# Kernel tuning notes

Hardware: AMD Instinct MI355X
Metric: run time of the kernel (lower is better)

The kernel has to match this reference:

```python
import jax, jax.numpy as jnp
import numpy as np

B, S, T = 32, 128, 64
H = 512
VS = VT = 32000


def _lstm_cell(x, h, c, W, U, b):
    # Keras LSTM gate order: i, f, g(cell), o
    z = x @ W + h @ U + b
    i, f, g, o = jnp.split(z, 4, axis=-1)
    c = jax.nn.sigmoid(f) * c + jax.nn.sigmoid(i) * jnp.tanh(g)
    h = jax.nn.sigmoid(o) * jnp.tanh(c)
    return h, c


def _lstm_scan(xs, h0, c0, W, U, b):
    # xs: [S, B, D]
    def step(carry, x):
        h, c = _lstm_cell(x, carry[0], carry[1], W, U, b)
        return (h, c), h
    (hT, cT), hs = jax.lax.scan(step, (h0, c0), xs)
    return hs, hT, cT


def setup_inputs() -> dict:
    key = jax.random.key(0)
    ks = jax.random.split(key, 16)
    def n(k, shape, s=0.02):
        return (jax.random.normal(k, shape, jnp.float32) * s).astype(jnp.float32)
    return {
        "src": jax.random.randint(ks[0], (B, S), 0, VS, jnp.int32),
        "trg": jax.random.randint(ks[1], (B, T), 0, VT, jnp.int32),
        "E_src": n(ks[2], (VS, H)),
        "E_trg": n(ks[3], (VT, H)),
        "Wf": n(ks[4], (H, 4 * H)), "Uf": n(ks[5], (H, 4 * H)), "bf": jnp.zeros((4 * H,), jnp.float32),
        "Wb": n(ks[6], (H, 4 * H)), "Ub": n(ks[7], (H, 4 * H)), "bb": jnp.zeros((4 * H,), jnp.float32),
        "Wd": n(ks[8], (H, 4 * H)), "Ud": n(ks[9], (H, 4 * H)), "bd": jnp.zeros((4 * H,), jnp.float32),
        "fcW": n(ks[10], (2 * H, H)), "fcb": jnp.zeros((H,), jnp.float32),
        "clsW": n(ks[11], (2 * H, VT)), "clsb": jnp.zeros((VT,), jnp.float32),
    }


def reference(src, trg, E_src, E_trg, Wf, Uf, bf, Wb, Ub, bb, Wd, Ud, bd, fcW, fcb, clsW, clsb):
    Bn = src.shape[0]
    Hn = E_src.shape[1]
    # --- Encoder: bidirectional LSTM ---
    xs = E_src[src].transpose(1, 0, 2)          # [S, B, H]
    z0 = jnp.zeros((Bn, Hn), xs.dtype)
    hs_f, hf, cf = _lstm_scan(xs, z0, z0, Wf, Uf, bf)
    hs_b, hb, cb = _lstm_scan(xs[::-1], z0, z0, Wb, Ub, bb)
    src_hidden = jnp.concatenate([hs_f, hs_b[::-1]], axis=-1).transpose(1, 0, 2)  # [B, S, 2H]
    # --- shared fc projections (same Dense, 2H -> H) ---
    src_h = src_hidden @ fcW + fcb                                   # [B, S, H]
    prev_h = jnp.concatenate([hf, hb], axis=-1) @ fcW + fcb          # [B, H]
    prev_c = jnp.concatenate([cf, cb], axis=-1) @ fcW + fcb          # [B, H]
    neg = jnp.where(src == 0, jnp.float32(-1e9), jnp.float32(0.0))   # [B, S]
    # --- Decoder (teacher forcing): per-step LSTM cell + dot-product attention ---
    ys = E_trg[trg[:, :-1]].transpose(1, 0, 2)  # [T-1, B, H]

    def step(carry, x):
        h, c = _lstm_cell(x, carry[0], carry[1], Wd, Ud, bd)
        score = jnp.einsum('bh,bsh->bs', h, src_h) + neg
        attn = jax.nn.softmax(score, axis=-1)
        ws = jnp.einsum('bs,bsh->bh', attn, src_h)
        return (h, c), jnp.concatenate([ws, h], axis=-1)  # dec_state [B, 2H]

    _, dec = jax.lax.scan(step, (prev_h, prev_c), ys)     # [T-1, B, 2H]
    logits = dec.transpose(1, 0, 2) @ clsW + clsb          # [B, T-1, VT]
    return logits
```

## Files before the change

### kernel.cpp

```cpp
#include <hip/hip_runtime.h>
#include <hip/hip_bf16.h>
#include <stdint.h>
#include <string.h>

constexpr int cB = 32, cS = 128, cT = 64, cH = 512, cH4 = 2048, cVT = 32000, cTM1 = 63;

typedef __attribute__((ext_vector_type(8))) __bf16 bf16x8;
typedef __attribute__((ext_vector_type(4))) float f32x4;

__device__ __forceinline__ float sigm(float x) { return 1.0f / (1.0f + expf(-x)); }

__device__ __forceinline__ bf16x8 sc_load16(const __hip_bfloat16* p) {
  bf16x8 r;
  asm volatile("global_load_dwordx4 %0, %1, off sc0 sc1"
               : "=&v"(r) : "v"(p) : "memory");
  return r;
}
__device__ __forceinline__ void sc_store4(__hip_bfloat16* p, unsigned v) {
  asm volatile("global_store_dword %0, %1, off sc0 sc1"
               :: "v"(p), "v"(v) : "memory");
}
__device__ __forceinline__ void pl_store4(__hip_bfloat16* p, unsigned v) {
  asm volatile("global_store_dword %0, %1, off"
               :: "v"(p), "v"(v) : "memory");
}
__device__ __forceinline__ unsigned sc_loadu(const unsigned* p) {
  unsigned r;
  asm volatile("global_load_dword %0, %1, off sc0 sc1"
               : "=&v"(r) : "v"(p) : "memory");
  asm volatile("s_waitcnt vmcnt(0)" ::: "memory");
  return r;
}
__device__ __forceinline__ void sc_storeu(unsigned* p, unsigned v) {
  asm volatile("global_store_dword %0, %1, off sc0 sc1"
               :: "v"(p), "v"(v) : "memory");
}

__global__ __launch_bounds__(64) void k_init_bars(unsigned* p) {
  p[threadIdx.x] = 0u;
}

__global__ __launch_bounds__(128) void k_embed_src(const int* __restrict__ src,
                                                   const float* __restrict__ E,
                                                   __hip_bfloat16* __restrict__ xs_bf,
                                                   float* __restrict__ neg) {
  int sb = blockIdx.x;
  int s = sb >> 5, b = sb & 31;
  int tok = src[b * cS + s];
  float4 e = ((const float4*)(E + (size_t)tok * cH))[threadIdx.x];
  __hip_bfloat16* drow = xs_bf + (size_t)sb * cH + threadIdx.x * 4;
  drow[0] = __float2bfloat16(e.x); drow[1] = __float2bfloat16(e.y);
  drow[2] = __float2bfloat16(e.z); drow[3] = __float2bfloat16(e.w);
  if (threadIdx.x == 0) neg[b * cS + s] = (tok == 0) ? -1e9f : 0.0f;
}

__global__ __launch_bounds__(128) void k_embed_trg(const int* __restrict__ trg,
                                                   const float* __restrict__ E,
                                                   __hip_bfloat16* __restrict__ ys_bf) {
  int tb = blockIdx.x;
  int t = tb >> 5, b = tb & 31;
  int tok = trg[b * cT + t];
  float4 e = ((const float4*)(E + (size_t)tok * cH))[threadIdx.x];
  __hip_bfloat16* drow = ys_bf + (size_t)tb * cH + threadIdx.x * 4;
  drow[0] = __float2bfloat16(e.x); drow[1] = __float2bfloat16(e.y);
  drow[2] = __float2bfloat16(e.z); drow[3] = __float2bfloat16(e.w);
}

__device__ __forceinline__ void f2bT_tile(const float* __restrict__ src,
                                          __hip_bfloat16* __restrict__ dst,
                                          int K, int N, int gi, int bx, int by,
                                          float (*t)[33]) {
  int nt = bx * 32, kt = by * 32;
  int c = threadIdx.x & 31, r0 = threadIdx.x >> 5;
#pragma unroll
  for (int i = 0; i < 4; ++i) {
    int r = r0 + i * 8;
    t[r][c] = src[(size_t)(kt + r) * N + nt + c];
  }
  __syncthreads();
#pragma unroll
  for (int i = 0; i < 4; ++i) {
    int row = nt + r0 + i * 8;
    int pr = gi ? (((row & 511) << 2) | (row >> 9)) : row;
    dst[(size_t)pr * K + kt + c] = __float2bfloat16(t[c][r0 + i * 8]);
  }
  __syncthreads();
}

__device__ __forceinline__ void f2bT_tile512(const float* __restrict__ src,
                                             __hip_bfloat16* __restrict__ dst,
                                             int K, int N, int bx, int by,
                                             float (*t)[33]) {
  int nt = bx * 32, kt = by * 32;
  int c = threadIdx.x & 31, r0 = (threadIdx.x >> 5) & 15;
#pragma unroll
  for (int i = 0; i < 2; ++i) {
    int r = r0 + i * 16;
    t[r][c] = src[(size_t)(kt + r) * N + nt + c];
  }
  __syncthreads();
#pragma unroll
  for (int i = 0; i < 2; ++i) {
    int row = nt + r0 + i * 16;
    dst[(size_t)row * K + kt + c] = __float2bfloat16(t[c][r0 + i * 16]);
  }
  __syncthreads();
}

__global__ __launch_bounds__(256) void k_prep(
    const float* __restrict__ Wf, const float* __restrict__ Wb, const float* __restrict__ Wd,
    const float* __restrict__ Uf, const float* __restrict__ Ub, const float* __restrict__ Ud,
    const float* __restrict__ fcW,
    const float* __restrict__ bf, const float* __restrict__ bb, const float* __restrict__ bd,
    __hip_bfloat16* __restrict__ Wtfx, __hip_bfloat16* __restrict__ Wtbx,
    __hip_bfloat16* __restrict__ Wtdx,
    __hip_bfloat16* __restrict__ Utf, __hip_bfloat16* __restrict__ Utb,
    __hip_bfloat16* __restrict__ Utd,
    __hip_bfloat16* __restrict__ fcWt,
    float* __restrict__ bfx, float* __restrict__ bbx, float* __restrict__ bdx,
    __hip_bfloat16* __restrict__ ys_pad) {
  __shared__ float t[32][33];
  int id = blockIdx.x;
  if (id < 6144) {
    int grp = id >> 10, r = id & 1023;
    const float* s; __hip_bfloat16* d;
    switch (grp) {
      case 0: s = Wf; d = Wtfx; break;
      case 1: s = Wb; d = Wtbx; break;
      case 2: s = Wd; d = Wtdx; break;
      case 3: s = Uf; d = Utf; break;
      case 4: s = Ub; d = Utb; break;
      default: s = Ud; d = Utd; break;
    }
    f2bT_tile(s, d, 512, 2048, 1, r & 63, r >> 6, t);
  } else if (id < 6656) {
    int r = id - 6144;
    f2bT_tile(fcW, fcWt, 1024, 512, 0, r & 15, r >> 4, t);
  } else if (id < 6680) {
    int r = id - 6656;
    const float* s = (r < 8) ? bf : ((r < 16) ? bb : bd);
    float* d = (r < 8) ? bfx : ((r < 16) ? bbx : bdx);
    int i = (r & 7) * 256 + threadIdx.x;
    d[i] = s[(i & 3) * 512 + (i >> 2)];
  } else {
    int r = id - 6680;
    ys_pad[r * 256 + threadIdx.x] = __float2bfloat16(0.0f);
  }
}

__global__ __launch_bounds__(256) void k_bgemm(const __hip_bfloat16* __restrict__ A,
                                               const __hip_bfloat16* __restrict__ Bt,
                                               const float* __restrict__ bias,
                                               float* __restrict__ C,
                                               int M, int K, int N) {
  __shared__ __hip_bfloat16 As[128 * 64];
  __shared__ __hip_bfloat16 Bs[128 * 64];
  const int tid = threadIdx.x;
  const int lane = tid & 63;
  const int wave = tid >> 6;
  const int wr = wave >> 1, wc = wave & 1;
  const int bm = blockIdx.x * 128, bn = blockIdx.y * 128;

  f32x4 acc[4][4] = {};

  const int srow = lane >> 3;
  const int scol = (lane & 7) * 8;

  for (int kt = 0; kt < K; kt += 64) {
#pragma unroll
    for (int i = 0; i < 4; ++i) {
      int c = wave * 4 + i;
      const __hip_bfloat16* ga = A + (size_t)(bm + c * 8 + srow) * K + kt + scol;
      __builtin_amdgcn_global_load_lds(
          (const __attribute__((address_space(1))) uint32_t*)ga,
          (__attribute__((address_space(3))) uint32_t*)(As + c * 512), 16, 0, 0);
      const __hip_bfloat16* gb = Bt + (size_t)(bn + c * 8 + srow) * K + kt + scol;
      __builtin_amdgcn_global_load_lds(
          (const __attribute__((address_space(1))) uint32_t*)gb,
          (__attribute__((address_space(3))) uint32_t*)(Bs + c * 512), 16, 0, 0);
    }
    __syncthreads();

#pragma unroll
    for (int kk = 0; kk < 64; kk += 32) {
      const int ko = kk + (lane >> 4) * 8;
      bf16x8 a[4], b[4];
      const int ar = wr * 64 + (lane & 15);
#pragma unroll
      for (int m = 0; m < 4; ++m)
        a[m] = *(const bf16x8*)(As + (size_t)(ar + m * 16) * 64 + ko);
      const int br = wc * 64 + (lane & 15);
#pragma unroll
      for (int n = 0; n < 4; ++n)
        b[n] = *(const bf16x8*)(Bs + (size_t)(br + n * 16) * 64 + ko);
#pragma unroll
      for (int m = 0; m < 4; ++m)
#pragma unroll
        for (int n = 0; n < 4; ++n)
          acc[m][n] = __builtin_amdgcn_mfma_f32_16x16x32_bf16(a[m], b[n], acc[m][n], 0, 0, 0);
    }
    __syncthreads();
  }

#pragma unroll
  for (int m = 0; m < 4; ++m) {
    const int row0 = bm + wr * 64 + m * 16 + (lane >> 4) * 4;
#pragma unroll
    for (int n = 0; n < 4; ++n) {
      const int col = bn + wc * 64 + n * 16 + (lane & 15);
      const float bv = bias[col];
#pragma unroll
      for (int r = 0; r < 4; ++r) {
        const int row = row0 + r;
        if (row < M) C[(size_t)row * N + col] = acc[m][n][r] + bv;
      }
    }
  }
}

#define SLOT_BARRIER(SLOTS, NB, GEN)                                             \
  {                                                                              \
    asm volatile("s_waitcnt vmcnt(2)" ::: "memory");                             \
    __builtin_amdgcn_sched_barrier(0);                                           \
    __builtin_amdgcn_s_barrier();                                                \
    if (tid == 0) sc_storeu((SLOTS) + (NB), (unsigned)(GEN));                    \
    if (wv == 0) {                                                               \
      for (;;) {                                                                 \
        unsigned v = sc_loadu((SLOTS) + (lane & 15));                            \
        if (__all((lane >= 16) | (v >= (unsigned)(GEN)))) break;                 \
        __builtin_amdgcn_s_sleep(1);                                             \
      }                                                                          \
    }                                                                            \
    __builtin_amdgcn_s_barrier();                                                \
    __builtin_amdgcn_sched_barrier(0);                                           \
  }

#define ENC_STEP(T, ZI0, ZI1, ZO0, ZO1)                                          \
  {                                                                              \
    const int t = (T);                                                           \
    const int trow = dir ? (127 - t) : t;                                        \
    if (t > 0) {                                                                 \
      const __hip_bfloat16* hsrc = hcur + (size_t)((t + 1) & 1) * 16384;         \
      bf16x8 hr[4];                                                              \
      _Pragma("unroll")                                                          \
      for (int i = 0; i < 4; ++i) {                                              \
        int c = tid + i * 512;                                                   \
        hr[i] = sc_load16(hsrc + (size_t)c * 8);                                 \
      }                                                                          \
      asm volatile("s_waitcnt vmcnt(0)" ::: "memory");                           \
      __builtin_amdgcn_sched_barrier(0);                                         \
      _Pragma("unroll")                                                          \
      for (int i = 0; i < 4; ++i) {                                              \
        int c = tid + i * 512;                                                   \
        int r = c >> 6, cc = (c & 63) * 8;                                       \
        *(bf16x8*)&Hs[r][cc] = hr[i];                                            \
      }                                                                          \
      asm volatile("s_waitcnt lgkmcnt(0)" ::: "memory");                         \
      __builtin_amdgcn_s_barrier();                                              \
      __builtin_amdgcn_sched_barrier(0);                                         \
    }                                                                            \
    f32x4 acc0 = {}, acc1 = {};                                                  \
    if (t > 0) {                                                                 \
      _Pragma("unroll")                                                          \
      for (int kk = 0; kk < 16; ++kk) {                                          \
        bf16x8 h0v = *(const bf16x8*)&Hs[b0][kk * 32 + fq * 8];                  \
        bf16x8 h1v = *(const bf16x8*)&Hs[b1][kk * 32 + fq * 8];                  \
        acc0 = __builtin_amdgcn_mfma_f32_16x16x32_bf16(afrag[kk], h0v, acc0, 0, 0, 0); \
        acc1 = __builtin_amdgcn_mfma_f32_16x16x32_bf16(afrag[kk], h1v, acc1, 0, 0, 0); \
      }                                                                          \
    }                                                                            \
    {                                                                            \
      float zi = ZI0[0] + acc0[0], zf = ZI0[1] + acc0[1],                        \
            zg = ZI0[2] + acc0[2], zo = ZI0[3] + acc0[3];                        \
      cs0 = sigm(zf) * cs0 + sigm(zi) * tanhf(zg);                               \
      Ho[b0][jloc] = __float2bfloat16(sigm(zo) * tanhf(cs0));                    \
    }                                                                            \
    {                                                                            \
      float zi = ZI1[0] + acc1[0], zf = ZI1[1] + acc1[1],                        \
            zg = ZI1[2] + acc1[2], zo = ZI1[3] + acc1[3];                        \
      cs1 = sigm(zf) * cs1 + sigm(zi) * tanhf(zg);                               \
      Ho[b1][jloc] = __float2bfloat16(sigm(zo) * tanhf(cs1));                    \
    }                                                                            \
    asm volatile("s_waitcnt lgkmcnt(0)" ::: "memory");                           \
    __builtin_amdgcn_s_barrier();                                                \
    __builtin_amdgcn_sched_barrier(0);                                           \
    {                                                                            \
      unsigned v = *(const unsigned*)&Ho[bb][jp];                                \
      sc_store4(hcur + (size_t)(t & 1) * 16384 + (size_t)bb * 512 + nb * 32 + jp, v); \
      pl_store4(hs + ((size_t)trow * 32 + bb) * 512 + nb * 32 + jp, v);          \
    }                                                                            \
    __builtin_amdgcn_sched_barrier(0);                                           \
    const int tn = (t < 127) ? t + 1 : 127;                                      \
    const int ntrow = dir ? (127 - tn) : tn;                                     \
    ZO0 = *(const f32x4*)(xW + ((size_t)(ntrow * 32 + b0)) * 2048 + zc);         \
    ZO1 = *(const f32x4*)(xW + ((size_t)(ntrow * 32 + b1)) * 2048 + zc);         \
    if (t < 127) SLOT_BARRIER(slots, nb, t + 1);                                 \
  }

__global__ __launch_bounds__(512, 1) void k_enc_mfma(
    const float* __restrict__ xWf, const float* __restrict__ xWb,
    const __hip_bfloat16* __restrict__ Utf, const __hip_bfloat16* __restrict__ Utb,
    __hip_bfloat16* __restrict__ hs_f, __hip_bfloat16* __restrict__ hs_b,
    __hip_bfloat16* __restrict__ henc,
    float* __restrict__ cf, float* __restrict__ cb,
    unsigned* bars) {
  __shared__ __hip_bfloat16 Hs[32][520];
  __shared__ __hip_bfloat16 Ho[32][36];

  const int bid = blockIdx.x;
  const int dir = bid >> 4, nb = bid & 15;
  const int c0 = nb * 128;
  const float* xW = dir ? xWb : xWf;
  const __hip_bfloat16* Ut = dir ? Utb : Utf;
  __hip_bfloat16* hs = dir ? hs_b : hs_f;
  __hip_bfloat16* hcur = henc + (size_t)dir * 32768;
  float* cOut = dir ? cb : cf;
  unsigned* slots = bars + dir * 16;

  const int tid = threadIdx.x;
  const int lane = tid & 63;
  const int wv = tid >> 6;
  const int fr = lane & 15;
  const int fq = lane >> 4;

  bf16x8 afrag[16];
#pragma unroll
  for (int kk = 0; kk < 16; ++kk)
    afrag[kk] = *(const bf16x8*)(Ut + (size_t)(c0 + wv * 16 + fr) * 512 + kk * 32 + fq * 8);

  const int jglob = nb * 32 + wv * 4 + fq;
  const int jloc = wv * 4 + fq;
  const int b0 = fr, b1 = fr + 16;
  const int zc = c0 + wv * 16 + fq * 4;
  const int bb = tid >> 4, jp = (tid & 15) * 2;
  float cs0 = 0.f, cs1 = 0.f;

  const int trow0 = dir ? 127 : 0;
  f32x4 zA0 = *(const f32x4*)(xW + ((size_t)(trow0 * 32 + b0)) * 2048 + zc);
  f32x4 zA1 = *(const f32x4*)(xW + ((size_t)(trow0 * 32 + b1)) * 2048 + zc);
  f32x4 zB0, zB1;

  for (int it = 0; it < 64; ++it) {
    ENC_STEP(2 * it, zA0, zA1, zB0, zB1);
    ENC_STEP(2 * it + 1, zB0, zB1, zA0, zA1);
  }
  cOut[(size_t)b0 * 512 + jglob] = cs0;
  cOut[(size_t)b1 * 512 + jglob] = cs1;
}

#define DEC_STEP(T, ZI0, ZI1, ZO0, ZO1)                                          \
  {                                                                              \
    const int t = (T);                                                           \
    if (t == 0) {                                                                \
      const float4* ph4 = (const float4*)prev_h;                                 \
      _Pragma("unroll")                                                          \
      for (int i = 0; i < 8; ++i) {                                              \
        int c = tid + i * 512;                                                   \
        float4 v = ph4[c];                                                       \
        int r = c >> 7, c4 = (c & 127) * 4;                                      \
        Hs[r][c4 + 0] = __float2bfloat16(v.x);                                   \
        Hs[r][c4 + 1] = __float2bfloat16(v.y);                                   \
        Hs[r][c4 + 2] = __float2bfloat16(v.z);                                   \
        Hs[r][c4 + 3] = __float2bfloat16(v.w);                                   \
      }                                                                          \
    } else {                                                                     \
      const __hip_bfloat16* hsrc = hdec + (size_t)((t + 1) & 1) * 16384;         \
      bf16x8 hr[4];                                                              \
      _Pragma("unroll")                                                          \
      for (int i = 0; i < 4; ++i) {                                              \
        int c = tid + i * 512;                                                   \
        hr[i] = sc_load16(hsrc + (size_t)c * 8);                                 \
      }                                                                          \
      asm volatile("s_waitcnt vmcnt(0)" ::: "memory");                           \
      __builtin_amdgcn_sched_barrier(0);                                         \
      _Pragma("unroll")                                                          \
      for (int i = 0; i < 4; ++i) {                                              \
        int c = tid + i * 512;                                                   \
        int r = c >> 6, cc = (c & 63) * 8;                                       \
        *(bf16x8*)&Hs[r][cc] = hr[i];                                            \
      }                                                                          \
    }                                                                            \
    asm volatile("s_waitcnt lgkmcnt(0)" ::: "memory");                           \
    __builtin_amdgcn_s_barrier();                                                \
    __builtin_amdgcn_sched_barrier(0);                                           \
    f32x4 acc0 = {}, acc1 = {};                                                  \
    _Pragma("unroll")                                                            \
    for (int kk = 0; kk < 16; ++kk) {                                            \
      bf16x8 h0v = *(const bf16x8*)&Hs[b0][kk * 32 + fq * 8];                    \
      bf16x8 h1v = *(const bf16x8*)&Hs[b1][kk * 32 + fq * 8];                    \
      acc0 = __builtin_amdgcn_mfma_f32_16x16x32_bf16(afrag[kk], h0v, acc0, 0, 0, 0); \
      acc1 = __builtin_amdgcn_mfma_f32_16x16x32_bf16(afrag[kk], h1v, acc1, 0, 0, 0); \
    }                                                                            \
    {                                                                            \
      float zi = ZI0[0] + acc0[0], zf = ZI0[1] + acc0[1],                        \
            zg = ZI0[2] + acc0[2], zo = ZI0[3] + acc0[3];                        \
      cs0 = sigm(zf) * cs0 + sigm(zi) * tanhf(zg);                               \
      Ho[b0][jloc] = __float2bfloat16(sigm(zo) * tanhf(cs0));                    \
    }                                                                            \
    {                                                                            \
      float zi = ZI1[0] + acc1[0], zf = ZI1[1] + acc1[1],                        \
            zg = ZI1[2] + acc1[2], zo = ZI1[3] + acc1[3];                        \
      cs1 = sigm(zf) * cs1 + sigm(zi) * tanhf(zg);                               \
      Ho[b1][jloc] = __float2bfloat16(sigm(zo) * tanhf(cs1));                    \
    }                                                                            \
    asm volatile("s_waitcnt lgkmcnt(0)" ::: "memory");                           \
    __builtin_amdgcn_s_barrier();                                                \
    __builtin_amdgcn_sched_barrier(0);                                           \
    {                                                                            \
      unsigned v = *(const unsigned*)&Ho[bb][jp];                                \
      sc_store4(hdec + (size_t)(t & 1) * 16384 + (size_t)bb * 512 + nb * 32 + jp, v); \
      pl_store4(decb + ((size_t)bb * cTM1 + t) * 1024 + 512 + nb * 32 + jp, v);  \
    }                                                                            \
    __builtin_amdgcn_sched_barrier(0);                                           \
    const int tn = (t < cTM1 - 1) ? t + 1 : cTM1 - 1;                            \
    ZO0 = *(const f32x4*)(yW + ((size_t)(tn * 32 + b0)) * 2048 + zc);            \
    ZO1 = *(const f32x4*)(yW + ((size_t)(tn * 32 + b1)) * 2048 + zc);            \
    if (t < cTM1 - 1) SLOT_BARRIER(slots, nb, t + 1);                            \
  }

__global__ __launch_bounds__(512, 1) void k_dec_mfma(
    const float* __restrict__ yW, const __hip_bfloat16* __restrict__ Utd,
    const float* __restrict__ prev_h, const float* __restrict__ prev_c,
    __hip_bfloat16* __restrict__ hdec, __hip_bfloat16* __restrict__ decb,
    const float* __restrict__ clsW, __hip_bfloat16* __restrict__ clsWt,
    unsigned* slots) {
  __shared__ __hip_bfloat16 Hs[32][520];
  __shared__ __hip_bfloat16 Ho[32][36];
  __shared__ float tcv[32][33];

  if (blockIdx.x >= 16) {
    for (int tile = blockIdx.x - 16; tile < 32000; tile += (int)gridDim.x - 16) {
      int bx = tile % 1000, by = tile / 1000;
      f2bT_tile512(clsW, clsWt, 1024, 32000, bx, by, tcv);
    }
    return;
  }

  const int nb = blockIdx.x;
  const int c0 = nb * 128;
  const int tid = threadIdx.x;
  const int lane = tid & 63;
  const int wv = tid >> 6;
  const int fr = lane & 15;
  const int fq = lane >> 4;

  bf16x8 afrag[16];
#pragma unroll
  for (int kk = 0; kk < 16; ++kk)
    afrag[kk] = *(const bf16x8*)(Utd + (size_t)(c0 + wv * 16 + fr) * 512 + kk * 32 + fq * 8);

  const int jglob = nb * 32 + wv * 4 + fq;
  const int jloc = wv * 4 + fq;
  const int b0 = fr, b1 = fr + 16;
  const int zc = c0 + wv * 16 + fq * 4;
  const int bb = tid >> 4, jp = (tid & 15) * 2;
  float cs0 = prev_c[(size_t)b0 * 512 + jglob];
  float cs1 = prev_c[(size_t)b1 * 512 + jglob];

  f32x4 zA0 = *(const f32x4*)(yW + ((size_t)b0) * 2048 + zc);
  f32x4 zA1 = *(const f32x4*)(yW + ((size_t)b1) * 2048 + zc);
  f32x4 zB0, zB1;

  for (int it = 0; it < 31; ++it) {
    DEC_STEP(2 * it, zA0, zA1, zB0, zB1);
    DEC_STEP(2 * it + 1, zB0, zB1, zA0, zA1);
  }
  DEC_STEP(62, zA0, zA1, zB0, zB1);
}

__global__ __launch_bounds__(128) void k_cat_bf(const __hip_bfloat16* __restrict__ hs_f,
                                                const __hip_bfloat16* __restrict__ hs_b,
                                                const float* __restrict__ cf,
                                                const float* __restrict__ cb,
                                                __hip_bfloat16* __restrict__ cat) {
  int r = blockIdx.x;
  int tid = threadIdx.x;
  __hip_bfloat16* drow = cat + (size_t)r * 1024 + tid * 8;
  if (r >= 4160) {
    bf16x8 zv = {};
    *(bf16x8*)drow = zv;
    return;
  }
  if (r < 4128) {
    const __hip_bfloat16 *pf, *pb;
    if (r < 4096) {
      int b = r >> 7, s = r & 127;
      pf = hs_f + ((size_t)s * 32 + b) * 512;
      pb = hs_b + ((size_t)s * 32 + b) * 512;
    } else {
      int b = r - 4096;
      pf = hs_f + ((size_t)127 * 32 + b) * 512;
      pb = hs_b + ((size_t)b) * 512;
    }
    const __hip_bfloat16* s8 = (tid < 64) ? (pf + tid * 8) : (pb + (tid - 64) * 8);
    *(bf16x8*)drow = *(const bf16x8*)s8;
  } else {
    int b = r - 4128;
    const float* s8 = (tid < 64) ? (cf + (size_t)b * 512 + tid * 8)
                                 : (cb + (size_t)b * 512 + (tid - 64) * 8);
    bf16x8 v;
#pragma unroll
    for (int i = 0; i < 8; ++i) v[i] = (__bf16)s8[i];
    *(bf16x8*)drow = v;
  }
}

__global__ __launch_bounds__(256) void k_attn_all(const float* __restrict__ src_h,
                                                  const float* __restrict__ neg,
                                                  __hip_bfloat16* __restrict__ decb) {
  int bid = blockIdx.x;
  int xcd = bid & 7, idx = bid >> 3;
  int b = xcd + 8 * (idx / 63);
  int t = idx % 63;
  int tx = threadIdx.x;
  __shared__ float hv[cH];
  __shared__ float part[256];
  __shared__ float sc[cS];
  __shared__ float red[cS];
  __hip_bfloat16* drow = decb + ((size_t)b * cTM1 + t) * (2 * cH);
  hv[tx] = __bfloat162float(drow[cH + tx]);
  hv[tx + 256] = __bfloat162float(drow[cH + tx + 256]);
  __syncthreads();
  {
    int s = tx >> 1, half = tx & 1;
    const float4* sr = (const float4*)(src_h + ((size_t)b * cS + s) * cH + half * 256);
    const float4* hh = (const float4*)(hv + half * 256);
    float acc = 0.f;
#pragma unroll 8
    for (int k = 0; k < 64; ++k) {
      float4 v = sr[k], h4 = hh[k];
      acc += v.x * h4.x + v.y * h4.y + v.z * h4.z + v.w * h4.w;
    }
    part[tx] = acc;
  }
  __syncthreads();
  if (tx < cS) {
    float s0 = part[2 * tx] + part[2 * tx + 1] + neg[b * cS + tx];
    sc[tx] = s0;
    red[tx] = s0;
  }
  __syncthreads();
  for (int off = 64; off >= 1; off >>= 1) {
    if (tx < off) red[tx] = fmaxf(red[tx], red[tx + off]);
    __syncthreads();
  }
  float mx = red[0];
  __syncthreads();
  float e = 0.f;
  if (tx < cS) { e = expf(sc[tx] - mx); red[tx] = e; }
  __syncthreads();
  for (int off = 64; off >= 1; off >>= 1) {
    if (tx < off) red[tx] += red[tx + off];
    __syncthreads();
  }
  float inv = 1.0f / red[0];
  __syncthreads();
  if (tx < cS) sc[tx] = e * inv;
  __syncthreads();
  float a0 = 0.f, a1 = 0.f;
  for (int s = 0; s < cS; ++s) {
    float w = sc[s];
    const float* sr = src_h + ((size_t)b * cS + s) * cH;
    a0 += w * sr[tx];
    a1 += w * sr[tx + 256];
  }
  drow[tx] = __float2bfloat16(a0);
  drow[tx + 256] = __float2bfloat16(a1);
}

extern "C" void kernel_launch(void* const* d_in, const int* in_sizes, int n_in,
                              void* d_out, int out_size, void* d_ws, size_t ws_size,
                              hipStream_t stream) {
  const int* src = (const int*)d_in[0];
  const int* trg = (const int*)d_in[1];
  const float* E_src = (const float*)d_in[2];
  const float* E_trg = (const float*)d_in[3];
  const float* Wf = (const float*)d_in[4];
  const float* Uf = (const float*)d_in[5];
  const float* bf = (const float*)d_in[6];
  const float* Wb = (const float*)d_in[7];
  const float* Ub = (const float*)d_in[8];
  const float* bb = (const float*)d_in[9];
  const float* Wd = (const float*)d_in[10];
  const float* Ud = (const float*)d_in[11];
  const float* bd = (const float*)d_in[12];
  const float* fcW = (const float*)d_in[13];
  const float* fcb = (const float*)d_in[14];
  const float* clsW = (const float*)d_in[15];
  const float* clsb = (const float*)d_in[16];
  float* out = (float*)d_out;
  float* ws = (float*)d_ws;

  float* xWf = ws;
  float* xWb = ws + 8388608;
  float* yW = ws + 16777216;
  __hip_bfloat16* hs_f = (__hip_bfloat16*)(ws + 20905984);
  __hip_bfloat16* hs_b = (__hip_bfloat16*)(ws + 21954560);
  float* cf = ws + 23003136;
  float* cb = ws + 23019520;
  float* neg = ws + 23035904;
  float* fco = ws + 23040000;
  __hip_bfloat16* decb = (__hip_bfloat16*)(ws + 25169920);
  __hip_bfloat16* Utd = (__hip_bfloat16*)(ws + 26218496);
  __hip_bfloat16* henc = (__hip_bfloat16*)(ws + 26742784);
  __hip_bfloat16* hdec = (__hip_bfloat16*)(ws + 26808320);
  unsigned* bars = (unsigned*)(ws + 26841088);
  float* pool = ws + 26841152;

  __hip_bfloat16* xs_bf = (__hip_bfloat16*)pool;
  __hip_bfloat16* ys_bf = (__hip_bfloat16*)(pool + 1048576);
  __hip_bfloat16* Utf = (__hip_bfloat16*)(pool + 1572864);
  __hip_bfloat16* Utb = (__hip_bfloat16*)(pool + 2097152);
  __hip_bfloat16* Wtfx = (__hip_bfloat16*)(pool + 2621440);
  __hip_bfloat16* Wtbx = (__hip_bfloat16*)(pool + 3145728);
  __hip_bfloat16* Wtdx = (__hip_bfloat16*)(pool + 3670016);
  float* bfx = pool + 4194304;
  float* bbx = pool + 4196352;
  float* bdx = pool + 4198400;
  __hip_bfloat16* fcWt = (__hip_bfloat16*)(pool + 4200448);
  __hip_bfloat16* cat_bf = (__hip_bfloat16*)pool;
  __hip_bfloat16* clsWt = (__hip_bfloat16*)xWf;

  k_embed_src<<<4096, 128, 0, stream>>>(src, E_src, xs_bf, neg);
  k_embed_trg<<<2016, 128, 0, stream>>>(trg, E_trg, ys_bf);
  k_prep<<<6744, 256, 0, stream>>>(Wf, Wb, Wd, Uf, Ub, Ud, fcW, bf, bb, bd,
                                   Wtfx, Wtbx, Wtdx, Utf, Utb, Utd, fcWt,
                                   bfx, bbx, bdx, ys_bf + (size_t)2016 * 512);

  k_bgemm<<<dim3(32, 16), 256, 0, stream>>>(xs_bf, Wtfx, bfx, xWf, 4096, 512, 2048);
  k_bgemm<<<dim3(32, 16), 256, 0, stream>>>(xs_bf, Wtbx, bbx, xWb, 4096, 512, 2048);
  k_bgemm<<<dim3(16, 16), 256, 0, stream>>>(ys_bf, Wtdx, bdx, yW, 2016, 512, 2048);

  k_init_bars<<<1, 64, 0, stream>>>(bars);
  k_enc_mfma<<<32, 512, 0, stream>>>(xWf, xWb, Utf, Utb, hs_f, hs_b, henc, cf, cb, bars);

  k_cat_bf<<<4224, 128, 0, stream>>>(hs_f, hs_b, cf, cb, cat_bf);
  k_bgemm<<<dim3(33, 4), 256, 0, stream>>>(cat_bf, fcWt, fcb, fco, 4160, 1024, 512);

  const float* prev_h = fco + (size_t)4096 * 512;
  const float* prev_c = fco + (size_t)4128 * 512;
  k_dec_mfma<<<256, 512, 0, stream>>>(yW, Utd, prev_h, prev_c, hdec, decb,
                                      clsW, clsWt, bars + 32);
  k_attn_all<<<2016, 256, 0, stream>>>(fco, neg, decb);

  k_bgemm<<<dim3(16, 250), 256, 0, stream>>>(decb, clsWt, clsb, out, 2016, 1024, 32000);
}
```

Measured before the change: 1.208 ms.

## Overlap decoder attention with recurrence and write encoder states straight into concat buffer

The encoder now stores each hidden state directly into the [B,S,2H] concatenated bf16 buffer, so the full k_cat_bf repack is replaced by a small tail kernel that handles only the final-state rows. The separate attention kernel is removed. After the 240 spare blocks of the decoder kernel finish transposing the classifier weights, they poll the per-step slot counters and compute attention for each (t,b) as soon as that step's hidden state is published. This hides attention behind the serial decoder recurrence, at the cost of coherent sc0/sc1 stores for decoder outputs, spin-waiting, and a narrower per-block attention loop.

```diff
diff --git a/kernel.cpp b/kernel.cpp
--- a/kernel.cpp
+++ b/kernel.cpp
@@ -13,6 +13,12 @@
 __device__ __forceinline__ bf16x8 sc_load16(const __hip_bfloat16* p) {
   bf16x8 r;
   asm volatile("global_load_dwordx4 %0, %1, off sc0 sc1"
+               : "=&v"(r) : "v"(p) : "memory");
+  return r;
+}
+__device__ __forceinline__ unsigned sc_load4u(const __hip_bfloat16* p) {
+  unsigned r;
+  asm volatile("global_load_dword %0, %1, off sc0 sc1"
                : "=&v"(r) : "v"(p) : "memory");
   return r;
 }
@@ -287,7 +293,7 @@
     {                                                                            \
       unsigned v = *(const unsigned*)&Ho[bb][jp];                                \
       sc_store4(hcur + (size_t)(t & 1) * 16384 + (size_t)bb * 512 + nb * 32 + jp, v); \
-      pl_store4(hs + ((size_t)trow * 32 + bb) * 512 + nb * 32 + jp, v);          \
+      pl_store4(catb + ((size_t)(bb * 128 + trow)) * 1024 + dhalf + nb * 32 + jp, v); \
     }                                                                            \
     __builtin_amdgcn_sched_barrier(0);                                           \
     const int tn = (t < 127) ? t + 1 : 127;                                      \
@@ -300,7 +306,7 @@
 __global__ __launch_bounds__(512, 1) void k_enc_mfma(
     const float* __restrict__ xWf, const float* __restrict__ xWb,
     const __hip_bfloat16* __restrict__ Utf, const __hip_bfloat16* __restrict__ Utb,
-    __hip_bfloat16* __restrict__ hs_f, __hip_bfloat16* __restrict__ hs_b,
+    __hip_bfloat16* __restrict__ catb,
     __hip_bfloat16* __restrict__ henc,
     float* __restrict__ cf, float* __restrict__ cb,
     unsigned* bars) {
@@ -312,7 +318,7 @@
   const int c0 = nb * 128;
   const float* xW = dir ? xWb : xWf;
   const __hip_bfloat16* Ut = dir ? Utb : Utf;
-  __hip_bfloat16* hs = dir ? hs_b : hs_f;
+  const int dhalf = dir * 512;
   __hip_bfloat16* hcur = henc + (size_t)dir * 32768;
   float* cOut = dir ? cb : cf;
   unsigned* slots = bars + dir * 16;
@@ -346,6 +352,62 @@
   }
   cOut[(size_t)b0 * 512 + jglob] = cs0;
   cOut[(size_t)b1 * 512 + jglob] = cs1;
+}
+
+__device__ void attn_one(const float* __restrict__ src_h, const float* __restrict__ neg,
+                         __hip_bfloat16* __restrict__ decb, int b, int t,
+                         float* hv, float* sc, float* red) {
+  const int tx = threadIdx.x;
+  __hip_bfloat16* drow = decb + ((size_t)b * cTM1 + t) * 1024;
+  if (tx < 256) {
+    unsigned u = sc_load4u(drow + 512 + tx * 2);
+    asm volatile("s_waitcnt vmcnt(0)" ::: "memory");
+    hv[tx * 2] = __uint_as_float(u << 16);
+    hv[tx * 2 + 1] = __uint_as_float(u & 0xffff0000u);
+  }
+  __syncthreads();
+  {
+    int s = tx >> 2, q = tx & 3;
+    const float4* sr = (const float4*)(src_h + ((size_t)b * cS + s) * cH + q * 128);
+    const float4* hh = (const float4*)(hv + q * 128);
+    float acc = 0.f;
+#pragma unroll 8
+    for (int k = 0; k < 32; ++k) {
+      float4 v = sr[k], h4 = hh[k];
+      acc += v.x * h4.x + v.y * h4.y + v.z * h4.z + v.w * h4.w;
+    }
+    acc += __shfl_xor(acc, 1);
+    acc += __shfl_xor(acc, 2);
+    if (q == 0) {
+      float s0 = acc + neg[b * cS + s];
+      sc[s] = s0;
+      red[s] = s0;
+    }
+  }
+  __syncthreads();
+  for (int off = 64; off >= 1; off >>= 1) {
+    if (tx < off) red[tx] = fmaxf(red[tx], red[tx + off]);
+    __syncthreads();
+  }
+  float mx = red[0];
+  __syncthreads();
+  float e = 0.f;
+  if (tx < cS) { e = expf(sc[tx] - mx); red[tx] = e; }
+  __syncthreads();
+  for (int off = 64; off >= 1; off >>= 1) {
+    if (tx < off) red[tx] += red[tx + off];
+    __syncthreads();
+  }
+  float inv = 1.0f / red[0];
+  __syncthreads();
+  if (tx < cS) sc[tx] = e * inv;
+  __syncthreads();
+  {
+    float a = 0.f;
+    const float* sr = src_h + (size_t)b * cS * cH + tx;
+    for (int s = 0; s < cS; ++s) a += sc[s] * sr[(size_t)s * cH];
+    drow[tx] = __float2bfloat16(a);
+  }
 }
 
 #define DEC_STEP(T, ZI0, ZI1, ZO0, ZO1)                                          \
@@ -409,7 +471,7 @@
     {                                                                            \
       unsigned v = *(const unsigned*)&Ho[bb][jp];                                \
       sc_store4(hdec + (size_t)(t & 1) * 16384 + (size_t)bb * 512 + nb * 32 + jp, v); \
-      pl_store4(decb + ((size_t)bb * cTM1 + t) * 1024 + 512 + nb * 32 + jp, v);  \
+      sc_store4(decb + ((size_t)bb * cTM1 + t) * 1024 + 512 + nb * 32 + jp, v);  \
     }                                                                            \
     __builtin_amdgcn_sched_barrier(0);                                           \
     const int tn = (t < cTM1 - 1) ? t + 1 : cTM1 - 1;                            \
@@ -423,24 +485,46 @@
     const float* __restrict__ prev_h, const float* __restrict__ prev_c,
     __hip_bfloat16* __restrict__ hdec, __hip_bfloat16* __restrict__ decb,
     const float* __restrict__ clsW, __hip_bfloat16* __restrict__ clsWt,
+    const float* __restrict__ src_h, const float* __restrict__ neg,
     unsigned* slots) {
   __shared__ __hip_bfloat16 Hs[32][520];
   __shared__ __hip_bfloat16 Ho[32][36];
   __shared__ float tcv[32][33];
-
-  if (blockIdx.x >= 16) {
-    for (int tile = blockIdx.x - 16; tile < 32000; tile += (int)gridDim.x - 16) {
-      int bx = tile % 1000, by = tile / 1000;
-      f2bT_tile512(clsW, clsWt, 1024, 32000, bx, by, tcv);
-    }
-    return;
-  }
-
-  const int nb = blockIdx.x;
-  const int c0 = nb * 128;
+  __shared__ float hv_sh[512];
+  __shared__ float sc_sh[128];
+  __shared__ float red_sh[128];
+
   const int tid = threadIdx.x;
   const int lane = tid & 63;
   const int wv = tid >> 6;
+
+  if (blockIdx.x >= 16) {
+    const int sidx = blockIdx.x - 16;
+    for (int tile = sidx; tile < 32000; tile += 240) {
+      f2bT_tile512(clsW, clsWt, 1024, 32000, tile % 1000, tile / 1000, tcv);
+    }
+    unsigned waited = 0;
+    for (int i = sidx; i < 2016; i += 240) {
+      int t = i >> 5, b = i & 31;
+      unsigned need = (unsigned)(t + 1);
+      if (need > waited) {
+        if (wv == 0) {
+          for (;;) {
+            unsigned v = sc_loadu(slots + (lane & 15));
+            if (__all((lane >= 16) | (v >= need))) break;
+            __builtin_amdgcn_s_sleep(4);
+          }
+        }
+        __syncthreads();
+        waited = need;
+      }
+      attn_one(src_h, neg, decb, b, t, hv_sh, sc_sh, red_sh);
+    }
+    return;
+  }
+
+  const int nb = blockIdx.x;
+  const int c0 = nb * 128;
   const int fr = lane & 15;
   const int fq = lane >> 4;
 
@@ -466,14 +550,15 @@
     DEC_STEP(2 * it + 1, zB0, zB1, zA0, zA1);
   }
   DEC_STEP(62, zA0, zA1, zB0, zB1);
-}
-
-__global__ __launch_bounds__(128) void k_cat_bf(const __hip_bfloat16* __restrict__ hs_f,
-                                                const __hip_bfloat16* __restrict__ hs_b,
-                                                const float* __restrict__ cf,
-                                                const float* __restrict__ cb,
-                                                __hip_bfloat16* __restrict__ cat) {
-  int r = blockIdx.x;
+  asm volatile("s_waitcnt vmcnt(0)" ::: "memory");
+  __builtin_amdgcn_s_barrier();
+  if (tid == 0) sc_storeu(slots + nb, (unsigned)cTM1);
+}
+
+__global__ __launch_bounds__(128) void k_cat_tail(const float* __restrict__ cf,
+                                                  const float* __restrict__ cb,
+                                                  __hip_bfloat16* __restrict__ cat) {
+  int r = 4096 + blockIdx.x;
   int tid = threadIdx.x;
   __hip_bfloat16* drow = cat + (size_t)r * 1024 + tid * 8;
   if (r >= 4160) {
@@ -482,16 +567,9 @@
     return;
   }
   if (r < 4128) {
-    const __hip_bfloat16 *pf, *pb;
-    if (r < 4096) {
-      int b = r >> 7, s = r & 127;
-      pf = hs_f + ((size_t)s * 32 + b) * 512;
-      pb = hs_b + ((size_t)s * 32 + b) * 512;
-    } else {
-      int b = r - 4096;
-      pf = hs_f + ((size_t)127 * 32 + b) * 512;
-      pb = hs_b + ((size_t)b) * 512;
-    }
+    int b = r - 4096;
+    const __hip_bfloat16* pf = cat + ((size_t)(b * 128 + 127)) * 1024;
+    const __hip_bfloat16* pb = cat + ((size_t)(b * 128 + 0)) * 1024 + 512;
     const __hip_bfloat16* s8 = (tid < 64) ? (pf + tid * 8) : (pb + (tid - 64) * 8);
     *(bf16x8*)drow = *(const bf16x8*)s8;
   } else {
@@ -503,69 +581,6 @@
     for (int i = 0; i < 8; ++i) v[i] = (__bf16)s8[i];
     *(bf16x8*)drow = v;
   }
-}
-
-__global__ __launch_bounds__(256) void k_attn_all(const float* __restrict__ src_h,
-                                                  const float* __restrict__ neg,
-                                                  __hip_bfloat16* __restrict__ decb) {
-  int bid = blockIdx.x;
-  int xcd = bid & 7, idx = bid >> 3;
-  int b = xcd + 8 * (idx / 63);
-  int t = idx % 63;
-  int tx = threadIdx.x;
-  __shared__ float hv[cH];
-  __shared__ float part[256];
-  __shared__ float sc[cS];
-  __shared__ float red[cS];
-  __hip_bfloat16* drow = decb + ((size_t)b * cTM1 + t) * (2 * cH);
-  hv[tx] = __bfloat162float(drow[cH + tx]);
-  hv[tx + 256] = __bfloat162float(drow[cH + tx + 256]);
-  __syncthreads();
-  {
-    int s = tx >> 1, half = tx & 1;
-    const float4* sr = (const float4*)(src_h + ((size_t)b * cS + s) * cH + half * 256);
-    const float4* hh = (const float4*)(hv + half * 256);
-    float acc = 0.f;
-#pragma unroll 8
-    for (int k = 0; k < 64; ++k) {
-      float4 v = sr[k], h4 = hh[k];
-      acc += v.x * h4.x + v.y * h4.y + v.z * h4.z + v.w * h4.w;
-    }
-    part[tx] = acc;
-  }
-  __syncthreads();
-  if (tx < cS) {
-    float s0 = part[2 * tx] + part[2 * tx + 1] + neg[b * cS + tx];
-    sc[tx] = s0;
-    red[tx] = s0;
-  }
-  __syncthreads();
-  for (int off = 64; off >= 1; off >>= 1) {
-    if (tx < off) red[tx] = fmaxf(red[tx], red[tx + off]);
-    __syncthreads();
-  }
-  float mx = red[0];
-  __syncthreads();
-  float e = 0.f;
-  if (tx < cS) { e = expf(sc[tx] - mx); red[tx] = e; }
-  __syncthreads();
-  for (int off = 64; off >= 1; off >>= 1) {
-    if (tx < off) red[tx] += red[tx + off];
-    __syncthreads();
-  }
-  float inv = 1.0f / red[0];
-  __syncthreads();
-  if (tx < cS) sc[tx] = e * inv;
-  __syncthreads();
-  float a0 = 0.f, a1 = 0.f;
-  for (int s = 0; s < cS; ++s) {
-    float w = sc[s];
-    const float* sr = src_h + ((size_t)b * cS + s) * cH;
-    a0 += w * sr[tx];
-    a1 += w * sr[tx + 256];
-  }
-  drow[tx] = __float2bfloat16(a0);
-  drow[tx + 256] = __float2bfloat16(a1);
 }
 
 extern "C" void kernel_launch(void* const* d_in, const int* in_sizes, int n_in,
@@ -594,8 +609,6 @@
   float* xWf = ws;
   float* xWb = ws + 8388608;
   float* yW = ws + 16777216;
-  __hip_bfloat16* hs_f = (__hip_bfloat16*)(ws + 20905984);
-  __hip_bfloat16* hs_b = (__hip_bfloat16*)(ws + 21954560);
   float* cf = ws + 23003136;
   float* cb = ws + 23019520;
   float* neg = ws + 23035904;
@@ -618,7 +631,7 @@
   float* bbx = pool + 4196352;
   float* bdx = pool + 4198400;
   __hip_bfloat16* fcWt = (__hip_bfloat16*)(pool + 4200448);
-  __hip_bfloat16* cat_bf = (__hip_bfloat16*)pool;
+  __hip_bfloat16* cat_bf = (__hip_bfloat16*)(pool + 4462592);
   __hip_bfloat16* clsWt = (__hip_bfloat16*)xWf;
 
   k_embed_src<<<4096, 128, 0, stream>>>(src, E_src, xs_bf, neg);
@@ -632,16 +645,15 @@
   k_bgemm<<<dim3(16, 16), 256, 0, stream>>>(ys_bf, Wtdx, bdx, yW, 2016, 512, 2048);
 
   k_init_bars<<<1, 64, 0, stream>>>(bars);
-  k_enc_mfma<<<32, 512, 0, stream>>>(xWf, xWb, Utf, Utb, hs_f, hs_b, henc, cf, cb, bars);
-
-  k_cat_bf<<<4224, 128, 0, stream>>>(hs_f, hs_b, cf, cb, cat_bf);
+  k_enc_mfma<<<32, 512, 0, stream>>>(xWf, xWb, Utf, Utb, cat_bf, henc, cf, cb, bars);
+
+  k_cat_tail<<<128, 128, 0, stream>>>(cf, cb, cat_bf);
   k_bgemm<<<dim3(33, 4), 256, 0, stream>>>(cat_bf, fcWt, fcb, fco, 4160, 1024, 512);
 
   const float* prev_h = fco + (size_t)4096 * 512;
   const float* prev_c = fco + (size_t)4128 * 512;
   k_dec_mfma<<<256, 512, 0, stream>>>(yW, Utd, prev_h, prev_c, hdec, decb,
-                                      clsW, clsWt, bars + 32);
-  k_attn_all<<<2016, 256, 0, stream>>>(fco, neg, decb);
+                                      clsW, clsWt, fco, neg, bars + 32);
 
   k_bgemm<<<dim3(16, 250), 256, 0, stream>>>(decb, clsWt, clsb, out, 2016, 1024, 32000);
 }
```

Measured after the change: 1.174 ms. 2.8% less time.
